# Kernel optimization log

Measured on AMD Instinct MI355X. Metric: run time of the kernel, lower is better.

Reference implementation:

```python
import jax, jax.numpy as jnp
import numpy as np

B, T = 32, 1024
VOCAB, N_POS = 300, 3001
D, N_HEAD, D_HID, L = 256, 2, 1024, 4
K1_PAD = 4  # kernel 9, padding 4; second conv is kernel 1, padding 0
EPS = 1e-5


def layer_norm(x, g, b):
    m = jnp.mean(x, axis=-1, keepdims=True)
    v = jnp.mean((x - m) ** 2, axis=-1, keepdims=True)
    return (x - m) * jax.lax.rsqrt(v + EPS) * g + b


def setup_inputs() -> dict:
    key = jax.random.key(0)
    ks = jax.random.split(key, 16)
    src_seq = jax.random.randint(ks[0], (B, T), 0, VOCAB)
    src_pos = jnp.broadcast_to(jnp.arange(1, T + 1), (B, T)).astype(jnp.int32)
    word_emb = (0.02 * jax.random.normal(ks[1], (VOCAB, D))).at[0].set(0.0)  # padding_idx=0
    pos_emb = (0.02 * jax.random.normal(ks[2], (N_POS, D))).at[0].set(0.0)
    s = 0.02
    qkv_w = np.sqrt(2.0 / (D + D // N_HEAD)) * jax.random.normal(ks[3], (L, 3 * D, D))
    qkv_b = jnp.zeros((L, 3 * D))
    fc_w = s * jax.random.normal(ks[4], (L, D, D))
    fc_b = jnp.zeros((L, D))
    ln1_g = jnp.ones((L, D)); ln1_b = jnp.zeros((L, D))
    conv1_w = s * jax.random.normal(ks[5], (L, D_HID, D, 9))
    conv1_b = jnp.zeros((L, D_HID))
    conv2_w = s * jax.random.normal(ks[6], (L, D, D_HID, 1))
    conv2_b = jnp.zeros((L, D))
    ln2_g = jnp.ones((L, D)); ln2_b = jnp.zeros((L, D))
    return dict(src_seq=src_seq, src_pos=src_pos, word_emb=word_emb, pos_emb=pos_emb,
                qkv_w=qkv_w, qkv_b=qkv_b, fc_w=fc_w, fc_b=fc_b,
                ln1_g=ln1_g, ln1_b=ln1_b, conv1_w=conv1_w, conv1_b=conv1_b,
                conv2_w=conv2_w, conv2_b=conv2_b, ln2_g=ln2_g, ln2_b=ln2_b)


def encoder(src_seq, src_pos, word_emb, pos_emb, qkv_w, qkv_b, fc_w, fc_b,
            ln1_g, ln1_b, conv1_w, conv1_b, conv2_w, conv2_b, ln2_g, ln2_b):
    non_pad = (src_seq != 0).astype(jnp.float32)[..., None]          # [B,T,1]
    key_pad = (src_seq == 0)[:, None, None, :]                        # [B,1,1,T]
    x = word_emb[src_seq] + pos_emb[src_pos]                          # [B,T,D]
    dk = D // N_HEAD

    def block(x, p):
        qw, qb, fw, fb, g1, be1, w1, b1, w2, b2, g2, be2 = p
        res = x
        h = layer_norm(x, g1, be1)
        qkv = h @ qw.T + qb                                           # [B,T,3D]
        q, k, v = jnp.split(qkv, 3, axis=-1)
        split = lambda t: t.reshape(B, T, N_HEAD, dk).transpose(0, 2, 1, 3)
        q, k, v = split(q), split(k), split(v)
        attn = jnp.einsum('bhqd,bhkd->bhqk', q, k) / jnp.sqrt(jnp.float32(dk))
        attn = jnp.where(key_pad, -jnp.inf, attn)
        attn = jax.nn.softmax(attn, axis=-1)
        o = jnp.einsum('bhqk,bhkd->bhqd', attn, v)
        o = o.transpose(0, 2, 1, 3).reshape(B, T, D)
        x = (o @ fw.T + fb) + res
        x = x * non_pad
        # position-wise conv FFN
        res = x
        h = layer_norm(x, g2, be2).transpose(0, 2, 1)                 # [B,D,T]
        h = jax.lax.conv_general_dilated(h, w1, (1,), [(K1_PAD, K1_PAD)],
                                         dimension_numbers=('NCH', 'OIH', 'NCH'))
        h = jax.nn.relu(h + b1[None, :, None])
        h = jax.lax.conv_general_dilated(h, w2, (1,), [(0, 0)],
                                         dimension_numbers=('NCH', 'OIH', 'NCH'))
        h = h + b2[None, :, None]
        x = h.transpose(0, 2, 1) + res
        x = x * non_pad
        return x, None

    params = (qkv_w, qkv_b, fc_w, fc_b, ln1_g, ln1_b,
              conv1_w, conv1_b, conv2_w, conv2_b, ln2_g, ln2_b)
    x, _ = jax.lax.scan(block, x, params)
    return x, non_pad


def reference(src_seq, src_pos, word_emb, pos_emb, qkv_w, qkv_b, fc_w, fc_b,
              ln1_g, ln1_b, conv1_w, conv1_b, conv2_w, conv2_b, ln2_g, ln2_b):
    return encoder(src_seq, src_pos, word_emb, pos_emb, qkv_w, qkv_b, fc_w, fc_b,
                   ln1_g, ln1_b, conv1_w, conv1_b, conv2_w, conv2_b, ln2_g, ln2_b)
```

## Files before the change

### kernel.cpp

```cpp
#include <hip/hip_runtime.h>


#define B_ 32
#define T_ 1024
#define D_ 256
#define NH_ 2
#define DK_ 128
#define DH_ 1024
#define L_ 4
#define MROWS (B_ * T_)
#define KCONV (D_ * 9)
#define TPAD 1032

typedef unsigned short u16;
typedef short bf16x8 __attribute__((ext_vector_type(8)));
typedef float f32x4 __attribute__((ext_vector_type(4)));
typedef u16 u16x8 __attribute__((ext_vector_type(8)));

__device__ __forceinline__ float bf2f(u16 h) {
    union { unsigned int u; float f; } a;
    a.u = ((unsigned int)h) << 16;
    return a.f;
}

__device__ __forceinline__ u16 f2bf(float f) {
    union { float f; unsigned int u; } a;
    a.f = f;
    unsigned int r = a.u + 0x7fffu + ((a.u >> 16) & 1u);
    return (u16)(r >> 16);
}

__device__ __forceinline__ void glds16(const u16* g, u16* l) {
    __builtin_amdgcn_global_load_lds(
        (const __attribute__((address_space(1))) void*)g,
        (__attribute__((address_space(3))) void*)l, 16, 0, 0);
}

__global__ void detect_kernel(const void* wemb_raw, int* flag) {
    __shared__ int cnt;
    if (threadIdx.x == 0) cnt = 0;
    __syncthreads();
    const u16* p = (const u16*)wemb_raw;
    if (p[256 + threadIdx.x] != 0) atomicAdd(&cnt, 1);
    __syncthreads();
    if (threadIdx.x == 0) *flag = (cnt >= 128) ? 1 : 0;
}

__global__ void cvt_any_kernel(const void* __restrict__ src, u16* __restrict__ dst,
                               int n, const int* __restrict__ flag) {
    int i = blockIdx.x * 256 + threadIdx.x;
    if (i >= n) return;
    if (*flag) dst[i] = ((const u16*)src)[i];
    else       dst[i] = f2bf(((const float*)src)[i]);
}

__global__ void w1_reorder2_kernel(const float* __restrict__ srcf,
                                   const u16* __restrict__ srch,
                                   u16* __restrict__ out, int n,
                                   const int* __restrict__ flag) {
    int idx = blockIdx.x * 256 + threadIdx.x;
    if (idx >= n) return;
    int l  = idx / (DH_ * KCONV);
    int r  = idx % (DH_ * KCONV);
    int oc = r / KCONV;
    int kk = r % KCONV;
    int kpos = kk >> 8;
    int ic   = kk & 255;
    size_t si = (size_t)l * DH_ * D_ * 9 + (oc * D_ + ic) * 9 + kpos;
    out[idx] = (*flag) ? srch[si] : f2bf(srcf[si]);
}

__global__ void sentinel_kernel(void* out, int out_size) {
    int i = blockIdx.x * 256 + threadIdx.x;
    if (i < out_size) ((u16*)out)[i] = 0x42F6;
}


__global__ void embed_kernel(const int* __restrict__ seq, const int* __restrict__ pos,
                             const u16* __restrict__ wemb, const u16* __restrict__ pemb,
                             float* __restrict__ X, float* __restrict__ NP) {
    int row = blockIdx.x;
    int d   = threadIdx.x;
    int s = seq[row];
    int p = pos[row];
    X[(size_t)row * D_ + d] = bf2f(wemb[s * D_ + d]) + bf2f(pemb[p * D_ + d]);
    if (d == 0) NP[row] = (s != 0) ? 1.0f : 0.0f;
}

__global__ void zero_pad_kernel(u16* __restrict__ Hp, int nb) {
    int i = blockIdx.x * 256 + threadIdx.x;
    if (i >= nb * 8 * 256) return;
    int b = i / (8 * 256);
    int r = (i / 256) & 7;
    int d = i & 255;
    int row = (r < 4) ? r : (1024 + r);
    Hp[(size_t)(b * TPAD + row) * D_ + d] = 0;
}

__global__ __launch_bounds__(256)
void ln_kernel(const float* __restrict__ x, const u16* __restrict__ g,
               const u16* __restrict__ bta, u16* __restrict__ outp) {
    int wave = threadIdx.x >> 6, lane = threadIdx.x & 63;
    int row = blockIdx.x * 4 + wave;
    const float* xr = x + (size_t)row * D_;
    float4 v = *(const float4*)&xr[lane * 4];
    float s  = v.x + v.y + v.z + v.w;
    float s2 = v.x * v.x + v.y * v.y + v.z * v.z + v.w * v.w;
#pragma unroll
    for (int d = 1; d < 64; d <<= 1) {
        s  += __shfl_xor(s,  d, 64);
        s2 += __shfl_xor(s2, d, 64);
    }
    float m   = s * (1.0f / 256.0f);
    float var = s2 * (1.0f / 256.0f) - m * m;
    float rr  = rsqrtf(var + 1e-5f);
    size_t orow = (size_t)((row >> 10) * TPAD + 4 + (row & 1023)) * D_;
    float vv[4] = {v.x, v.y, v.z, v.w};
#pragma unroll
    for (int k = 0; k < 4; k++) {
        int d = lane * 4 + k;
        outp[orow + d] = f2bf((vv[k] - m) * rr * bf2f(g[d]) + bf2f(bta[d]));
    }
}

__global__ void out_kernel(const float* __restrict__ X, const float* __restrict__ NP,
                           void* __restrict__ out, int out_size,
                           const int* __restrict__ flag) {
    int i = blockIdx.x * 256 + threadIdx.x;
    if (i >= out_size) return;
    const int n1 = MROWS * D_;
    float v = (i < n1) ? X[i] : NP[i - n1];
    if (*flag) ((u16*)out)[i] = f2bf(v);
    else       ((float*)out)[i] = v;
}

template <int AMAP, int EPI, int K>
__global__ __launch_bounds__(256)
void gemm_mfma(const u16* __restrict__ A, const u16* __restrict__ W,
               const u16* __restrict__ bias, const float* __restrict__ resid,
               const float* __restrict__ mask, void* __restrict__ Cp,
               u16* __restrict__ vout, int M, int N) {
    __shared__ __align__(16) u16 As[128 * 64];
    __shared__ __align__(16) u16 Bs[128 * 64];
    const int tid  = threadIdx.x;
    const int wave = tid >> 6, lane = tid & 63;
    const int quad = lane >> 4, l15 = lane & 15;
    const int m0 = blockIdx.y * 128, n0 = blockIdx.x * 128;
    const int wm = (wave >> 1) * 64, wn = (wave & 1) * 64;
    const int srow = wave * 32;
    const int row8 = lane >> 3;
    const int grp  = ((lane & 7) ^ row8) * 8;
    f32x4 acc[4][4] = {};

    const u16* pa;
    {
        int m = m0 + srow + row8;
        if (AMAP == 0) pa = A + (size_t)m * K + grp;
        else {
            int hr = (m >> 10) * TPAD + (m & 1023) + (AMAP == 1 ? 4 : 0);
            pa = A + (size_t)hr * D_ + grp;
        }
    }
    const u16* pb = W + (size_t)(n0 + srow + row8) * K + grp;
    constexpr size_t rsA = (AMAP == 0) ? (size_t)K : (size_t)D_;
    constexpr size_t rsB = (size_t)K;

    u16* lda = &As[srow * 64];
    u16* ldb = &Bs[srow * 64];
    const int rg = (quad ^ (l15 & 7)) * 8;

    int kpos = 0;
    constexpr int nkt = K / 64;
    for (int t = 0; t < nkt; t++) {
#pragma unroll
        for (int q = 0; q < 4; q++) {
            glds16(pa + (size_t)q * 8 * rsA, lda + q * 8 * 64);
            glds16(pb + (size_t)q * 8 * rsB, ldb + q * 8 * 64);
        }
        if (AMAP == 2) {
            if (kpos == 8) { kpos = 0; pa += 64 - 8 * 256; pb += 64 - 8 * 256; }
            else           { kpos++;  pa += 256;           pb += 256; }
        } else { pa += 64; pb += 64; }
        __builtin_amdgcn_s_waitcnt(0);
        __syncthreads();
#pragma unroll
        for (int ks = 0; ks < 2; ks++) {
            bf16x8 af[4], bfr[4];
#pragma unroll
            for (int i = 0; i < 4; i++)
                af[i] = *(const bf16x8*)&As[(wm + i * 16 + l15) * 64 + (rg ^ (ks * 32))];
#pragma unroll
            for (int j = 0; j < 4; j++)
                bfr[j] = *(const bf16x8*)&Bs[(wn + j * 16 + l15) * 64 + (rg ^ (ks * 32))];
#pragma unroll
            for (int i = 0; i < 4; i++)
#pragma unroll
                for (int j = 0; j < 4; j++)
                    acc[i][j] = __builtin_amdgcn_mfma_f32_16x16x32_bf16(
                        af[i], bfr[j], acc[i][j], 0, 0, 0);
        }
        __syncthreads();
    }

    float bv[4];
#pragma unroll
    for (int j = 0; j < 4; j++) bv[j] = bf2f(bias[n0 + wn + j * 16 + l15]);
#pragma unroll
    for (int i = 0; i < 4; i++) {
#pragma unroll
        for (int j = 0; j < 4; j++) {
            int n = n0 + wn + j * 16 + l15;
            int mbase = m0 + wm + i * 16 + quad * 4;
            float o[4];
#pragma unroll
            for (int r = 0; r < 4; r++) {
                float v = acc[i][j][r] + bv[j];
                if (EPI == 1) v = fmaxf(v, 0.0f);
                o[r] = v;
            }
            if (EPI == 2) {
#pragma unroll
                for (int r = 0; r < 4; r++) {
                    int m = mbase + r;
                    float v = (o[r] + resid[(size_t)m * N + n]) * mask[m];
                    ((float*)Cp)[(size_t)m * N + n] = v;
                }
            } else if (EPI == 3) {
                if (n0 < 512) {
#pragma unroll
                    for (int r = 0; r < 4; r++)
                        ((u16*)Cp)[(size_t)(mbase + r) * 512 + n] = f2bf(o[r]);
                } else {
                    int dg = n - 512;
                    int bb = mbase >> 10, tt = mbase & 1023;
                    ushort4 pk;
                    pk.x = f2bf(o[0]); pk.y = f2bf(o[1]);
                    pk.z = f2bf(o[2]); pk.w = f2bf(o[3]);
                    *(ushort4*)&vout[(size_t)((dg >> 7) + (bb << 1)) * (128 * 1024)
                                     + (size_t)(dg & 127) * 1024 + tt] = pk;
                }
            } else {
#pragma unroll
                for (int r = 0; r < 4; r++)
                    ((u16*)Cp)[(size_t)(mbase + r) * N + n] = f2bf(o[r]);
            }
        }
    }
}

__global__ __launch_bounds__(256, 2)
void attn_mfma(const u16* __restrict__ QKV, const u16* __restrict__ Vg,
               const float* __restrict__ NPg, u16* __restrict__ Hp) {
    __shared__ __align__(16) u16 Ks[64 * 128];
    __shared__ __align__(16) u16 Vt[128 * 64];
    __shared__ __align__(16) u16 Ps[4 * 32 * 72];
    __shared__ float npS[1024];
    const int tid  = threadIdx.x;
    const int wave = tid >> 6, lane = tid & 63;
    const int quad = lane >> 4, l15 = lane & 15;
    const int hb = blockIdx.x;
    const int h = hb & (NH_ - 1), b = hb >> 1;
    const int t0 = blockIdx.y * 128;
    const float scale = 0.08838834764831845f;
    u16* Psw = Ps + wave * 32 * 72;
    const u16* Vgh = Vg + (size_t)hb * (128 * 1024);

    for (int i = tid; i < 1024; i += 256) npS[i] = NPg[b * 1024 + i];

    bf16x8 q_a[2][4];
#pragma unroll
    for (int sub = 0; sub < 2; sub++)
#pragma unroll
        for (int s = 0; s < 4; s++)
            q_a[sub][s] = *(const bf16x8*)(QKV
                + (size_t)(b * 1024 + t0 + sub * 64 + wave * 16 + l15) * 512
                + h * DK_ + s * 32 + quad * 8);

    float m_st[2][4], l_st[2][4];
    f32x4 oacc[2][8] = {};
#pragma unroll
    for (int sub = 0; sub < 2; sub++)
#pragma unroll
        for (int r = 0; r < 4; r++) { m_st[sub][r] = -1e30f; l_st[sub][r] = 0.0f; }

    for (int kk = 0; kk < 16; kk++) {
        const int k0 = kk * 64;
        if (kk) __syncthreads();
#pragma unroll
        for (int i = 0; i < 4; i++) {
            int c = i * 256 + tid;
            int key = c >> 4, gk = (c & 15) ^ (key & 15);
            glds16(QKV + (size_t)(b * 1024 + k0 + key) * 512 + 256 + h * DK_ + gk * 8,
                   Ks + (size_t)(i * 256 + wave * 64) * 8);
            int d = c >> 3, gv = (c & 7) ^ (d & 7);
            glds16(Vgh + (size_t)d * 1024 + k0 + gv * 8,
                   Vt + (size_t)(i * 256 + wave * 64) * 8);
        }
        __builtin_amdgcn_s_waitcnt(0);
        __syncthreads();

        f32x4 s4[2][4] = {};
#pragma unroll
        for (int nt = 0; nt < 4; nt++) {
#pragma unroll
            for (int s = 0; s < 4; s++) {
                bf16x8 kb = *(const bf16x8*)&Ks[(nt * 16 + l15) * 128
                                                + ((s * 4 + quad) ^ l15) * 8];
                s4[0][nt] = __builtin_amdgcn_mfma_f32_16x16x32_bf16(
                    q_a[0][s], kb, s4[0][nt], 0, 0, 0);
                s4[1][nt] = __builtin_amdgcn_mfma_f32_16x16x32_bf16(
                    q_a[1][s], kb, s4[1][nt], 0, 0, 0);
            }
        }

#pragma unroll
        for (int sub = 0; sub < 2; sub++) {
#pragma unroll
            for (int nt = 0; nt < 4; nt++) {
                bool pad = (npS[k0 + nt * 16 + l15] == 0.0f);
#pragma unroll
                for (int r = 0; r < 4; r++)
                    s4[sub][nt][r] = pad ? -1e30f : s4[sub][nt][r] * scale;
            }
            float alpha[4];
#pragma unroll
            for (int r = 0; r < 4; r++) {
                float v = fmaxf(fmaxf(s4[sub][0][r], s4[sub][1][r]),
                                fmaxf(s4[sub][2][r], s4[sub][3][r]));
#pragma unroll
                for (int d = 1; d < 16; d <<= 1) v = fmaxf(v, __shfl_xor(v, d, 64));
                float mnew = fmaxf(m_st[sub][r], v);
                alpha[r] = __expf(m_st[sub][r] - mnew);
                m_st[sub][r] = mnew;
                l_st[sub][r] *= alpha[r];
            }
#pragma unroll
            for (int nt = 0; nt < 4; nt++)
#pragma unroll
                for (int r = 0; r < 4; r++)
                    s4[sub][nt][r] = __expf(s4[sub][nt][r] - m_st[sub][r]);
#pragma unroll
            for (int r = 0; r < 4; r++) {
                float v = s4[sub][0][r] + s4[sub][1][r] + s4[sub][2][r] + s4[sub][3][r];
#pragma unroll
                for (int d = 1; d < 16; d <<= 1) v += __shfl_xor(v, d, 64);
                l_st[sub][r] += v;
            }
#pragma unroll
            for (int dt = 0; dt < 8; dt++)
#pragma unroll
                for (int r = 0; r < 4; r++) oacc[sub][dt][r] *= alpha[r];
#pragma unroll
            for (int nt = 0; nt < 4; nt++)
#pragma unroll
                for (int r = 0; r < 4; r++)
                    Psw[(sub * 16 + quad * 4 + r) * 72 + nt * 16 + l15] =
                        f2bf(s4[sub][nt][r]);
        }

#pragma unroll
        for (int ks = 0; ks < 2; ks++) {
            bf16x8 pa0 = *(const bf16x8*)&Psw[l15 * 72 + ks * 32 + quad * 8];
            bf16x8 pa1 = *(const bf16x8*)&Psw[(16 + l15) * 72 + ks * 32 + quad * 8];
#pragma unroll
            for (int dt = 0; dt < 8; dt++) {
                int d = dt * 16 + l15;
                bf16x8 vb = *(const bf16x8*)&Vt[d * 64
                                                + (((ks * 4 + quad) ^ (d & 7)) * 8)];
                oacc[0][dt] = __builtin_amdgcn_mfma_f32_16x16x32_bf16(
                    pa0, vb, oacc[0][dt], 0, 0, 0);
                oacc[1][dt] = __builtin_amdgcn_mfma_f32_16x16x32_bf16(
                    pa1, vb, oacc[1][dt], 0, 0, 0);
            }
        }
    }

#pragma unroll
    for (int sub = 0; sub < 2; sub++)
#pragma unroll
        for (int r = 0; r < 4; r++) {
            float inv = 1.0f / l_st[sub][r];
            int t = t0 + sub * 64 + wave * 16 + quad * 4 + r;
            size_t orow = (size_t)(b * TPAD + 4 + t) * D_ + h * DK_;
#pragma unroll
            for (int dt = 0; dt < 8; dt++)
                Hp[orow + dt * 16 + l15] = f2bf(oacc[sub][dt][r] * inv);
        }
}


static inline int cdiv(int a, int b) { return (a + b - 1) / b; }

extern "C" void kernel_launch(void* const* d_in, const int* in_sizes, int n_in,
                              void* d_out, int out_size, void* d_ws, size_t ws_size,
                              hipStream_t stream) {
    const int* seq = (const int*)d_in[0];
    const int* pos = (const int*)d_in[1];
    (void)in_sizes; (void)n_in;

    int   cb = 8, w1L = 1;
    int*   FLAG; float* X; float* NP; u16* Hpad; u16* SCR; u16* W1R;
    u16 *WEMB, *PEMB, *QKVW, *QKVB, *FCW, *FCB, *G1c, *B1c, *C1B, *C2W, *C2B, *G2c, *B2c;

    unsigned char* wsb = (unsigned char*)d_ws;
    size_t off;
    auto build = [&](int cb_, int w1L_) -> size_t {
        off = 0;
        auto take = [&](size_t bytes) {
            unsigned char* p = wsb + off;
            off += (bytes + 255) & ~(size_t)255;
            return p;
        };
        FLAG = (int*)  take(4);
        X    = (float*)take((size_t)MROWS * D_ * 4);
        NP   = (float*)take((size_t)MROWS * 4);
        Hpad = (u16*)  take((size_t)cb_ * TPAD * D_ * 2);
        SCR  = (u16*)  take((size_t)cb_ * T_ * DH_ * 2);
        W1R  = (u16*)  take((size_t)w1L_ * DH_ * KCONV * 2);
        WEMB = (u16*)  take((size_t)300 * D_ * 2);
        PEMB = (u16*)  take((size_t)3001 * D_ * 2);
        QKVW = (u16*)  take((size_t)L_ * 3 * D_ * D_ * 2);
        QKVB = (u16*)  take((size_t)L_ * 3 * D_ * 2);
        FCW  = (u16*)  take((size_t)L_ * D_ * D_ * 2);
        FCB  = (u16*)  take((size_t)L_ * D_ * 2);
        G1c  = (u16*)  take((size_t)L_ * D_ * 2);
        B1c  = (u16*)  take((size_t)L_ * D_ * 2);
        C1B  = (u16*)  take((size_t)L_ * DH_ * 2);
        C2W  = (u16*)  take((size_t)L_ * D_ * DH_ * 2);
        C2B  = (u16*)  take((size_t)L_ * D_ * 2);
        G2c  = (u16*)  take((size_t)L_ * D_ * 2);
        B2c  = (u16*)  take((size_t)L_ * D_ * 2);
        return off;
    };
    if      (build(32, L_) <= ws_size) { cb = 32; w1L = L_; }
    else if (build(8,  L_) <= ws_size) { cb = 8;  w1L = L_; }
    else if (build(8,  1)  <= ws_size) { cb = 8;  w1L = 1;  }
    else {
        sentinel_kernel<<<cdiv(out_size, 256), 256, 0, stream>>>(d_out, out_size);
        return;
    }
    const int nch = B_ / cb;
    const int Mc  = cb * T_;

    detect_kernel<<<1, 256, 0, stream>>>(d_in[2], FLAG);
    auto cvt = [&](const void* src, u16* dst, int n) {
        cvt_any_kernel<<<cdiv(n, 256), 256, 0, stream>>>(src, dst, n, FLAG);
    };
    cvt(d_in[2],  WEMB, 300 * D_);
    cvt(d_in[3],  PEMB, 3001 * D_);
    cvt(d_in[4],  QKVW, L_ * 3 * D_ * D_);
    cvt(d_in[5],  QKVB, L_ * 3 * D_);
    cvt(d_in[6],  FCW,  L_ * D_ * D_);
    cvt(d_in[7],  FCB,  L_ * D_);
    cvt(d_in[8],  G1c,  L_ * D_);
    cvt(d_in[9],  B1c,  L_ * D_);
    cvt(d_in[11], C1B,  L_ * DH_);
    cvt(d_in[12], C2W,  L_ * D_ * DH_);
    cvt(d_in[13], C2B,  L_ * D_);
    cvt(d_in[14], G2c,  L_ * D_);
    cvt(d_in[15], B2c,  L_ * D_);
    if (w1L == L_) {
        int n = L_ * DH_ * KCONV;
        w1_reorder2_kernel<<<cdiv(n, 256), 256, 0, stream>>>(
            (const float*)d_in[10], (const u16*)d_in[10], W1R, n, FLAG);
    }

    embed_kernel<<<MROWS, 256, 0, stream>>>(seq, pos, WEMB, PEMB, X, NP);
    zero_pad_kernel<<<cb * 8, 256, 0, stream>>>(Hpad, cb);

    for (int l = 0; l < L_; l++) {
        for (int c = 0; c < nch; c++) {
            const size_t ro = (size_t)c * Mc;
            u16* QKV = SCR;
            u16* Vg  = SCR + (size_t)Mc * 512;
            ln_kernel<<<Mc / 4, 256, 0, stream>>>(
                X + ro * D_, G1c + l * D_, B1c + l * D_, Hpad);
            gemm_mfma<1, 3, 256><<<dim3(6, Mc / 128), 256, 0, stream>>>(
                Hpad, QKVW + (size_t)l * 3 * D_ * D_, QKVB + l * 3 * D_,
                nullptr, nullptr, QKV, Vg, Mc, 768);
            attn_mfma<<<dim3(NH_ * cb, 8), 256, 0, stream>>>(
                QKV, Vg, NP + ro, Hpad);
            gemm_mfma<1, 2, 256><<<dim3(2, Mc / 128), 256, 0, stream>>>(
                Hpad, FCW + (size_t)l * D_ * D_, FCB + l * D_,
                X + ro * D_, NP + ro, X + ro * D_, nullptr, Mc, D_);
        }
        const u16* w1p = W1R + (w1L == L_ ? (size_t)l * DH_ * KCONV : 0);
        if (w1L != L_) {
            int n = DH_ * KCONV;
            w1_reorder2_kernel<<<cdiv(n, 256), 256, 0, stream>>>(
                (const float*)d_in[10] + (size_t)l * DH_ * D_ * 9,
                (const u16*)d_in[10] + (size_t)l * DH_ * D_ * 9,
                W1R, n, FLAG);
        }
        for (int c = 0; c < nch; c++) {
            const size_t ro = (size_t)c * Mc;
            ln_kernel<<<Mc / 4, 256, 0, stream>>>(
                X + ro * D_, G2c + l * D_, B2c + l * D_, Hpad);
            gemm_mfma<2, 1, 2304><<<dim3(8, Mc / 128), 256, 0, stream>>>(
                Hpad, w1p, C1B + l * DH_,
                nullptr, nullptr, SCR, nullptr, Mc, DH_);
            gemm_mfma<0, 2, 1024><<<dim3(2, Mc / 128), 256, 0, stream>>>(
                SCR, C2W + (size_t)l * D_ * DH_, C2B + l * D_,
                X + ro * D_, NP + ro, X + ro * D_, nullptr, Mc, D_);
        }
    }

    out_kernel<<<cdiv(out_size, 256), 256, 0, stream>>>(X, NP, d_out, out_size, FLAG);
}
```

Measured before the change: 1.568 ms.

## Add 256x256-tile 8-wave conv1 GEMM kernel with interleaved LDS prefetch

```diff
diff --git a/kernel.cpp b/kernel.cpp
--- a/kernel.cpp
+++ b/kernel.cpp
@@ -11,6 +11,7 @@
 #define MROWS (B_ * T_)
 #define KCONV (D_ * 9)
 #define TPAD 1032
+#define NKT_C1 36
 
 typedef unsigned short u16;
 typedef short bf16x8 __attribute__((ext_vector_type(8)));
@@ -243,6 +244,154 @@
 #pragma unroll
                 for (int r = 0; r < 4; r++)
                     ((u16*)Cp)[(size_t)(mbase + r) * N + n] = f2bf(o[r]);
+            }
+        }
+    }
+}
+
+__global__ __launch_bounds__(512, 2)
+void gemm_conv1_8p(const u16* __restrict__ Ag, const u16* __restrict__ Wg,
+                   const u16* __restrict__ bias, u16* __restrict__ Cp) {
+    __shared__ __align__(16) u16 As[2][16384];
+    __shared__ __align__(16) u16 Bs[2][16384];
+    const int tid  = threadIdx.x;
+    const int lane = tid & 63;
+    const int wave = tid >> 6;
+    const int quad = lane >> 4, l15 = lane & 15;
+    const int wr = wave >> 2, wc = wave & 3;
+    const int m0 = blockIdx.y << 8, n0 = blockIdx.x << 8;
+    const int hr0 = (m0 >> 10) * TPAD + (m0 & 1023);
+    const int srow = tid >> 3, sch = tid & 7;
+
+    const u16* pA[4];
+    const u16* pB[4];
+#pragma unroll
+    for (int z = 0; z < 4; z++) {
+        int r  = z * 64 + srow;
+        int ch = (sch ^ (r & 7)) * 8;
+        pA[z] = Ag + (size_t)(hr0 + r) * 256 + ch;
+        pB[z] = Wg + (size_t)(n0 + r) * KCONV + ch;
+    }
+    const int ld0 = tid * 8;
+
+#pragma unroll
+    for (int z = 0; z < 4; z++) glds16(pA[z], &As[0][z * 4096 + ld0]);
+#pragma unroll
+    for (int z = 0; z < 4; z++) glds16(pB[z], &Bs[0][z * 4096 + ld0]);
+#pragma unroll
+    for (int z = 0; z < 4; z++) { pA[z] += 64; glds16(pA[z], &As[1][z * 4096 + ld0]); }
+
+    const int cA0  = (quad ^ (l15 & 7)) * 8;
+    const int cA1  = cA0 ^ 32;
+    const int arow = (wr * 128 + l15) * 64;
+    const int brow = (wc * 64  + l15) * 64;
+
+    f32x4 acc[8][4] = {};
+
+#pragma unroll 1
+    for (int t = 0; t < NKT_C1; t++) {
+        const int s = t & 1;
+        u16* AsS = As[s];
+        u16* BsS = Bs[s];
+        u16* AsP = As[s];
+        u16* BsP = Bs[s ^ 1];
+        bf16x8 a0[8], a1[8], b0, b1;
+
+        if (t < NKT_C1 - 1) asm volatile("s_waitcnt vmcnt(4)" ::: "memory");
+        else                asm volatile("s_waitcnt vmcnt(0)" ::: "memory");
+        __builtin_amdgcn_s_barrier();
+        asm volatile("" ::: "memory");
+#pragma unroll
+        for (int mf = 0; mf < 8; mf++)
+            a0[mf] = *(const bf16x8*)&AsS[arow + mf * 1024 + cA0];
+        b0 = *(const bf16x8*)&BsS[brow + cA0];
+        b1 = *(const bf16x8*)&BsS[brow + 1024 + cA0];
+        if (t + 1 < NKT_C1) {
+            pB[0] += 64; pB[1] += 64;
+            glds16(pB[0], &BsP[ld0]);
+            glds16(pB[1], &BsP[4096 + ld0]);
+        }
+        __builtin_amdgcn_s_setprio(1);
+#pragma unroll
+        for (int mf = 0; mf < 8; mf++) {
+            acc[mf][0] = __builtin_amdgcn_mfma_f32_16x16x32_bf16(a0[mf], b0, acc[mf][0], 0, 0, 0);
+            acc[mf][1] = __builtin_amdgcn_mfma_f32_16x16x32_bf16(a0[mf], b1, acc[mf][1], 0, 0, 0);
+        }
+        __builtin_amdgcn_s_setprio(0);
+        asm volatile("s_waitcnt lgkmcnt(0)" ::: "memory");
+        __builtin_amdgcn_s_barrier();
+        asm volatile("" ::: "memory");
+
+#pragma unroll
+        for (int mf = 0; mf < 8; mf++)
+            a1[mf] = *(const bf16x8*)&AsS[arow + mf * 1024 + cA1];
+        b0 = *(const bf16x8*)&BsS[brow + cA1];
+        b1 = *(const bf16x8*)&BsS[brow + 1024 + cA1];
+        if (t + 1 < NKT_C1) {
+            pB[2] += 64; pB[3] += 64;
+            glds16(pB[2], &BsP[2 * 4096 + ld0]);
+            glds16(pB[3], &BsP[3 * 4096 + ld0]);
+        }
+        __builtin_amdgcn_s_setprio(1);
+#pragma unroll
+        for (int mf = 0; mf < 8; mf++) {
+            acc[mf][0] = __builtin_amdgcn_mfma_f32_16x16x32_bf16(a1[mf], b0, acc[mf][0], 0, 0, 0);
+            acc[mf][1] = __builtin_amdgcn_mfma_f32_16x16x32_bf16(a1[mf], b1, acc[mf][1], 0, 0, 0);
+        }
+        __builtin_amdgcn_s_setprio(0);
+        asm volatile("s_waitcnt lgkmcnt(0)" ::: "memory");
+        __builtin_amdgcn_s_barrier();
+        asm volatile("" ::: "memory");
+
+        b0 = *(const bf16x8*)&BsS[brow + 2 * 1024 + cA0];
+        b1 = *(const bf16x8*)&BsS[brow + 3 * 1024 + cA0];
+        if (t + 2 < NKT_C1) {
+            pA[0] += 64; pA[1] += 64;
+            glds16(pA[0], &AsP[ld0]);
+            glds16(pA[1], &AsP[4096 + ld0]);
+        }
+        __builtin_amdgcn_s_setprio(1);
+#pragma unroll
+        for (int mf = 0; mf < 8; mf++) {
+            acc[mf][2] = __builtin_amdgcn_mfma_f32_16x16x32_bf16(a0[mf], b0, acc[mf][2], 0, 0, 0);
+            acc[mf][3] = __builtin_amdgcn_mfma_f32_16x16x32_bf16(a0[mf], b1, acc[mf][3], 0, 0, 0);
+        }
+        __builtin_amdgcn_s_setprio(0);
+        asm volatile("s_waitcnt lgkmcnt(0)" ::: "memory");
+        __builtin_amdgcn_s_barrier();
+        asm volatile("" ::: "memory");
+
+        b0 = *(const bf16x8*)&BsS[brow + 2 * 1024 + cA1];
+        b1 = *(const bf16x8*)&BsS[brow + 3 * 1024 + cA1];
+        if (t + 2 < NKT_C1) {
+            pA[2] += 64; pA[3] += 64;
+            glds16(pA[2], &AsP[2 * 4096 + ld0]);
+            glds16(pA[3], &AsP[3 * 4096 + ld0]);
+        }
+        __builtin_amdgcn_s_setprio(1);
+#pragma unroll
+        for (int mf = 0; mf < 8; mf++) {
+            acc[mf][2] = __builtin_amdgcn_mfma_f32_16x16x32_bf16(a1[mf], b0, acc[mf][2], 0, 0, 0);
+            acc[mf][3] = __builtin_amdgcn_mfma_f32_16x16x32_bf16(a1[mf], b1, acc[mf][3], 0, 0, 0);
+        }
+        __builtin_amdgcn_s_setprio(0);
+        asm volatile("s_waitcnt lgkmcnt(0)" ::: "memory");
+    }
+
+    float bv[4];
+#pragma unroll
+    for (int nf = 0; nf < 4; nf++)
+        bv[nf] = bf2f(bias[n0 + wc * 64 + nf * 16 + l15]);
+#pragma unroll
+    for (int mf = 0; mf < 8; mf++) {
+        const int mr = m0 + wr * 128 + mf * 16 + quad * 4;
+#pragma unroll
+        for (int nf = 0; nf < 4; nf++) {
+            const int cc = n0 + wc * 64 + nf * 16 + l15;
+#pragma unroll
+            for (int r = 0; r < 4; r++) {
+                float v = fmaxf(acc[mf][nf][r] + bv[nf], 0.0f);
+                Cp[(size_t)(mr + r) * 1024 + cc] = f2bf(v);
             }
         }
     }
@@ -496,9 +645,8 @@
             const size_t ro = (size_t)c * Mc;
             ln_kernel<<<Mc / 4, 256, 0, stream>>>(
                 X + ro * D_, G2c + l * D_, B2c + l * D_, Hpad);
-            gemm_mfma<2, 1, 2304><<<dim3(8, Mc / 128), 256, 0, stream>>>(
-                Hpad, w1p, C1B + l * DH_,
-                nullptr, nullptr, SCR, nullptr, Mc, DH_);
+            gemm_conv1_8p<<<dim3(4, Mc / 256), 512, 0, stream>>>(
+                Hpad, w1p, C1B + l * DH_, SCR);
             gemm_mfma<0, 2, 1024><<<dim3(2, Mc / 128), 256, 0, stream>>>(
                 SCR, C2W + (size_t)l * D_ * DH_, C2B + l * D_,
                 X + ro * D_, NP + ro, X + ro * D_, nullptr, Mc, D_);
```

Result: faster. 1.426 ms (-9.0%).

## Add dedicated conv1 GEMM kernel keeping full A window resident in LDS

Applied to the files above, without the earlier changes.

```diff
diff --git a/kernel.cpp b/kernel.cpp
--- a/kernel.cpp
+++ b/kernel.cpp
@@ -11,6 +11,7 @@
 #define MROWS (B_ * T_)
 #define KCONV (D_ * 9)
 #define TPAD 1032
+#define NKT_C1 36
 
 typedef unsigned short u16;
 typedef short bf16x8 __attribute__((ext_vector_type(8)));
@@ -243,6 +244,121 @@
 #pragma unroll
                 for (int r = 0; r < 4; r++)
                     ((u16*)Cp)[(size_t)(mbase + r) * N + n] = f2bf(o[r]);
+            }
+        }
+    }
+}
+
+__global__ __launch_bounds__(512, 2)
+void gemm_conv1_ar(const u16* __restrict__ Ag, const u16* __restrict__ Wg,
+                   const u16* __restrict__ bias, u16* __restrict__ Cp) {
+    __shared__ __align__(16) u16 Ap[264 * 256];
+    const int tid  = threadIdx.x;
+    const int lane = tid & 63;
+    const int wave = tid >> 6;
+    const int quad = lane >> 4, l15 = lane & 15;
+    const int wr = wave >> 2, wc = wave & 3;
+    int ntile, mtile;
+    if (gridDim.y == 128) {
+        const int f   = blockIdx.y * 4 + blockIdx.x;
+        const int xcd = f & 7, pos = f >> 3;
+        ntile = xcd >> 1;
+        mtile = ((xcd & 1) << 6) + pos;
+    } else { ntile = blockIdx.x; mtile = blockIdx.y; }
+    const int m0 = mtile << 8, n0 = ntile << 8;
+    const int hr0 = (m0 >> 10) * TPAD + (m0 & 1023);
+
+#pragma unroll
+    for (int k = 0; k < 16; k++) {
+        int c = k * 512 + tid;
+        int r = c >> 5, cc = c & 31;
+        glds16(Ag + (size_t)(hr0 + r) * 256 + ((cc ^ (r & 7)) * 8),
+               &Ap[(size_t)(k * 512 + wave * 64) * 8]);
+    }
+    if (tid < 256) {
+        int c = 8192 + tid;
+        int r = c >> 5, cc = c & 31;
+        glds16(Ag + (size_t)(hr0 + r) * 256 + ((cc ^ (r & 7)) * 8),
+               &Ap[(size_t)(8192 + wave * 64) * 8]);
+    }
+
+    const u16* pwB = Wg + (size_t)(n0 + wc * 64 + l15) * KCONV + quad * 8;
+    const u16* pn0 = pwB;
+    const u16* pn1 = pwB + 1 * 16 * KCONV;
+    const u16* pn2 = pwB + 2 * 16 * KCONV;
+    const u16* pn3 = pwB + 3 * 16 * KCONV;
+    const int arow_l = wr * 128 + l15;
+    f32x4 acc[8][4] = {};
+    bf16x8 bA[8], bB[8];
+
+#define LOADB(BS) do {                                                        \
+    BS[0] = *(const bf16x8*)pn0; BS[1] = *(const bf16x8*)(pn0 + 32); pn0 += 64; \
+    BS[2] = *(const bf16x8*)pn1; BS[3] = *(const bf16x8*)(pn1 + 32); pn1 += 64; \
+    BS[4] = *(const bf16x8*)pn2; BS[5] = *(const bf16x8*)(pn2 + 32); pn2 += 64; \
+    BS[6] = *(const bf16x8*)pn3; BS[7] = *(const bf16x8*)(pn3 + 32); pn3 += 64; \
+} while (0)
+
+#define TILE(T, BS) do {                                                      \
+    const int _ro  = (T) >> 2;                                                \
+    const int _swz = (l15 + _ro) & 7;                                         \
+    const int _c0  = ((((T) & 3) * 8 + quad) ^ _swz) * 8;                     \
+    const int _bse = (arow_l + _ro) * 256;                                    \
+    bf16x8 _a[8];                                                             \
+    _Pragma("unroll")                                                         \
+    for (int mf = 0; mf < 8; mf++)                                            \
+        _a[mf] = *(const bf16x8*)&Ap[_bse + mf * 4096 + _c0];                 \
+    __builtin_amdgcn_s_setprio(1);                                            \
+    _Pragma("unroll")                                                         \
+    for (int mf = 0; mf < 8; mf++) {                                          \
+        acc[mf][0] = __builtin_amdgcn_mfma_f32_16x16x32_bf16(_a[mf], BS[0], acc[mf][0], 0, 0, 0); \
+        acc[mf][1] = __builtin_amdgcn_mfma_f32_16x16x32_bf16(_a[mf], BS[2], acc[mf][1], 0, 0, 0); \
+        acc[mf][2] = __builtin_amdgcn_mfma_f32_16x16x32_bf16(_a[mf], BS[4], acc[mf][2], 0, 0, 0); \
+        acc[mf][3] = __builtin_amdgcn_mfma_f32_16x16x32_bf16(_a[mf], BS[6], acc[mf][3], 0, 0, 0); \
+    }                                                                         \
+    __builtin_amdgcn_s_setprio(0);                                            \
+    _Pragma("unroll")                                                         \
+    for (int mf = 0; mf < 8; mf++)                                            \
+        _a[mf] = *(const bf16x8*)&Ap[_bse + mf * 4096 + (_c0 ^ 32)];          \
+    __builtin_amdgcn_s_setprio(1);                                            \
+    _Pragma("unroll")                                                         \
+    for (int mf = 0; mf < 8; mf++) {                                          \
+        acc[mf][0] = __builtin_amdgcn_mfma_f32_16x16x32_bf16(_a[mf], BS[1], acc[mf][0], 0, 0, 0); \
+        acc[mf][1] = __builtin_amdgcn_mfma_f32_16x16x32_bf16(_a[mf], BS[3], acc[mf][1], 0, 0, 0); \
+        acc[mf][2] = __builtin_amdgcn_mfma_f32_16x16x32_bf16(_a[mf], BS[5], acc[mf][2], 0, 0, 0); \
+        acc[mf][3] = __builtin_amdgcn_mfma_f32_16x16x32_bf16(_a[mf], BS[7], acc[mf][3], 0, 0, 0); \
+    }                                                                         \
+    __builtin_amdgcn_s_setprio(0);                                            \
+} while (0)
+
+    LOADB(bA);
+    __builtin_amdgcn_s_waitcnt(0);
+    __syncthreads();
+
+#pragma unroll 1
+    for (int tt = 0; tt < NKT_C1; tt += 2) {
+        LOADB(bB);
+        TILE(tt, bA);
+        if (tt + 2 < NKT_C1) LOADB(bA);
+        TILE(tt + 1, bB);
+    }
+
+#undef LOADB
+#undef TILE
+
+    float bv[4];
+#pragma unroll
+    for (int nf = 0; nf < 4; nf++)
+        bv[nf] = bf2f(bias[n0 + wc * 64 + nf * 16 + l15]);
+#pragma unroll
+    for (int mf = 0; mf < 8; mf++) {
+        const int mr = m0 + wr * 128 + mf * 16 + quad * 4;
+#pragma unroll
+        for (int nf = 0; nf < 4; nf++) {
+            const int cc = n0 + wc * 64 + nf * 16 + l15;
+#pragma unroll
+            for (int r = 0; r < 4; r++) {
+                float v = fmaxf(acc[mf][nf][r] + bv[nf], 0.0f);
+                Cp[(size_t)(mr + r) * 1024 + cc] = f2bf(v);
             }
         }
     }
@@ -496,9 +612,8 @@
             const size_t ro = (size_t)c * Mc;
             ln_kernel<<<Mc / 4, 256, 0, stream>>>(
                 X + ro * D_, G2c + l * D_, B2c + l * D_, Hpad);
-            gemm_mfma<2, 1, 2304><<<dim3(8, Mc / 128), 256, 0, stream>>>(
-                Hpad, w1p, C1B + l * DH_,
-                nullptr, nullptr, SCR, nullptr, Mc, DH_);
+            gemm_conv1_ar<<<dim3(4, Mc / 256), 512, 0, stream>>>(
+                Hpad, w1p, C1B + l * DH_, SCR);
             gemm_mfma<0, 2, 1024><<<dim3(2, Mc / 128), 256, 0, stream>>>(
                 SCR, C2W + (size_t)l * D_ * DH_, C2B + l * D_,
                 X + ro * D_, NP + ro, X + ro * D_, nullptr, Mc, D_);
```

Result: slower. 1.972 ms (+25.8%).
